# Kernel optimization log

Hardware: AMD Instinct MI355X
Metric: run time of the kernel (lower is better)

The kernel has to match this reference:

```python
import jax, jax.numpy as jnp
import numpy as np

MARGIN = 10.0
EPS = 1e-8


def setup_inputs() -> dict:
    key = jax.random.key(0)
    k1, k2, k3 = jax.random.split(key, 3)
    V, B, C, D = 2, 16384, 100, 512
    feat = jax.random.normal(k1, (V, B, D), dtype=jnp.float32)
    label = jax.random.randint(k2, (B,), 0, C, dtype=jnp.int64)
    anchor = jax.random.normal(k3, (V, C, D), dtype=jnp.float32)
    return {"feat": feat, "label": label, "anchor": anchor}


def reference(feat, label, anchor):
    # feat: [V, B, D], label: [B], anchor: [V, C, D]
    V, B, D = feat.shape
    C = anchor.shape[1]

    # ----- per-view center loss + cosine similarity -----
    centers = anchor[:, label, :]                      # [V, B, D] gather
    diff = feat - centers
    center_loss = jnp.sum(diff * diff, axis=(1, 2)) / 2.0 / B   # [V]

    fn = jnp.maximum(jnp.linalg.norm(feat, axis=-1), EPS)        # [V, B]
    cn = jnp.maximum(jnp.linalg.norm(centers, axis=-1), EPS)     # [V, B]
    sims = jnp.sum(feat * centers, axis=-1) / (fn * cn)          # [V, B]

    # ----- inter-class margin loss (vectorized pairwise sq-dist) -----
    sq = jnp.sum(anchor * anchor, axis=-1)             # [V, C]
    gram = jnp.einsum('vcd,ved->vce', anchor, anchor)  # [V, C, C]
    pd = sq[:, :, None] + sq[:, None, :] - 2.0 * gram  # [V, C, C] squared dists
    # sum over i<j = (full sum - diagonal) / 2; diagonal is 0 analytically
    diag = jnp.einsum('vcc->v', pd)
    pair_sum = (jnp.sum(pd, axis=(1, 2)) - diag) * 0.5            # [V]
    inter = pair_sum / (C * (C - 1))
    inter_loss = jnp.maximum(MARGIN - inter, 0.0)                 # [V]

    loss = jnp.mean(center_loss) + jnp.mean(inter_loss)
    return loss, sims
```

## Files before the change

### kernel.cpp

```cpp
#include <hip/hip_runtime.h>
#include <math.h>

namespace {
constexpr int V = 2;
constexpr int B = 16384;
constexpr int C = 100;
constexpr int D = 512;
constexpr float MARGIN = 10.0f;
constexpr float EPS = 1e-8f;

constexpr int RB = 2048;
constexpr int ROWS_PER_WAVE = 4;
constexpr int IB_PER_V = 8;
constexpr int IB = V * IB_PER_V;
constexpr int CHUNK = 13;
}

__global__ __launch_bounds__(256) void main_kernel(
    const float* __restrict__ feat, const int* __restrict__ label,
    const float* __restrict__ anchor, float* __restrict__ sims,
    float* __restrict__ ws)
{
    __shared__ float blk[4];
    const int wave = threadIdx.x >> 6;
    const int lane = threadIdx.x & 63;

    if (blockIdx.x < RB) {
        const int wid = blockIdx.x * 4 + wave;
        float s_dd = 0.f;
#pragma unroll
        for (int r = 0; r < ROWS_PER_WAVE; ++r) {
            const int row = wid * ROWS_PER_WAVE + r;
            const int v = row >> 14;
            const int b = row & (B - 1);
            const float* frow = feat + (size_t)row * D;
            const float* crow = anchor + ((size_t)v * C + label[b]) * D;
            float s_ff = 0.f, s_cc = 0.f, s_fc = 0.f;
#pragma unroll
            for (int h = 0; h < 2; ++h) {
                const int d = h * 256 + lane * 4;
                const float4 f = *reinterpret_cast<const float4*>(frow + d);
                const float4 c = *reinterpret_cast<const float4*>(crow + d);
                s_ff += f.x*f.x + f.y*f.y + f.z*f.z + f.w*f.w;
                s_cc += c.x*c.x + c.y*c.y + c.z*c.z + c.w*c.w;
                s_fc += f.x*c.x + f.y*c.y + f.z*c.z + f.w*c.w;
                const float dx = f.x-c.x, dy = f.y-c.y, dz = f.z-c.z, dw = f.w-c.w;
                s_dd += dx*dx + dy*dy + dz*dz + dw*dw;
            }
#pragma unroll
            for (int off = 32; off; off >>= 1) {
                s_ff += __shfl_xor(s_ff, off);
                s_cc += __shfl_xor(s_cc, off);
                s_fc += __shfl_xor(s_fc, off);
            }
            if (lane == 0) {
                const float fn = fmaxf(sqrtf(s_ff), EPS);
                const float cn = fmaxf(sqrtf(s_cc), EPS);
                sims[row] = s_fc / (fn * cn);
            }
        }
#pragma unroll
        for (int off = 32; off; off >>= 1) s_dd += __shfl_xor(s_dd, off);
        if (lane == 0) blk[wave] = s_dd;
        __syncthreads();
        if (threadIdx.x == 0)
            ws[blockIdx.x] = blk[0] + blk[1] + blk[2] + blk[3];
    } else {
        const int ib = blockIdx.x - RB;
        const int v = ib >> 3, chunk = ib & 7;
        const int c0 = chunk * CHUNK;
        const int c1 = (c0 + CHUNK < C) ? c0 + CHUNK : C;
        const float* a = anchor + (size_t)v * C * D;
        const int d0 = threadIdx.x, d1 = threadIdx.x + 256;
        float m0 = 0.f, m1 = 0.f, s = 0.f;
        for (int c = c0; c < c1; ++c) {
            const float x0 = a[(size_t)c * D + d0];
            const float x1 = a[(size_t)c * D + d1];
            m0 += x0; m1 += x1; s += x0*x0 + x1*x1;
        }
        float* im = ws + RB + IB;
        im[ib * D + d0] = m0;
        im[ib * D + d1] = m1;
#pragma unroll
        for (int off = 32; off; off >>= 1) s += __shfl_xor(s, off);
        if (lane == 0) blk[wave] = s;
        __syncthreads();
        if (threadIdx.x == 0)
            ws[RB + ib] = blk[0] + blk[1] + blk[2] + blk[3];
    }
}

__global__ __launch_bounds__(1024) void finalize_kernel(
    const float* __restrict__ ws, float* __restrict__ out)
{
    const float* partials = ws;
    const float* is = ws + RB;
    const float* im = ws + RB + IB;
    const int t = threadIdx.x;
    const int wave = t >> 6, lane = t & 63;

    float sdd = partials[t] + partials[t + 1024];

    const int v = t >> 9, d = t & 511;
    float m = 0.f;
#pragma unroll
    for (int k = 0; k < IB_PER_V; ++k)
        m += im[((size_t)v * IB_PER_V + k) * D + d];
    float mm = m * m;

#pragma unroll
    for (int off = 32; off; off >>= 1) {
        sdd += __shfl_xor(sdd, off);
        mm  += __shfl_xor(mm, off);
    }
    __shared__ float rdd[16], rmm[16];
    if (lane == 0) { rdd[wave] = sdd; rmm[wave] = mm; }
    __syncthreads();
    if (t == 0) {
        float ddt = 0.f;
        for (int w = 0; w < 16; ++w) ddt += rdd[w];
        float MM0 = 0.f, MM1 = 0.f;
        for (int w = 0; w < 8;  ++w) MM0 += rmm[w];
        for (int w = 8; w < 16; ++w) MM1 += rmm[w];
        float S0 = 0.f, S1 = 0.f;
        for (int k = 0; k < IB_PER_V; ++k) { S0 += is[k]; S1 += is[IB_PER_V + k]; }
        const float denom = (float)(C * (C - 1));
        const float inter0 = ((float)C * S0 - MM0) / denom;
        const float inter1 = ((float)C * S1 - MM1) / denom;
        const float il = 0.5f * (fmaxf(MARGIN - inter0, 0.f) +
                                 fmaxf(MARGIN - inter1, 0.f));
        out[0] = ddt / (4.0f * (float)B) + il;
    }
}

extern "C" void kernel_launch(void* const* d_in, const int* in_sizes, int n_in,
                              void* d_out, int out_size, void* d_ws, size_t ws_size,
                              hipStream_t stream)
{
    const float* feat   = (const float*)d_in[0];
    const int*   label  = (const int*)d_in[1];
    const float* anchor = (const float*)d_in[2];
    float* out  = (float*)d_out;
    float* ws   = (float*)d_ws;
    float* sims = out + 1;

    hipLaunchKernelGGL(main_kernel, dim3(RB + IB), dim3(256), 0, stream,
                       feat, label, anchor, sims, ws);
    hipLaunchKernelGGL(finalize_kernel, dim3(1), dim3(1024), 0, stream,
                       ws, out);
}
```

Before: 98.35 us.

## Fuse finalize into main kernel via last-block atomic counter

Removes the separate single-block finalize kernel. The last block to finish, detected with an atomic counter and threadfences, now performs the final reduction. The inter-class anchor-sum work moves onto the first 16 row blocks instead of running in extra blocks. This saves one kernel launch and the gap between kernels, but adds a memset launch for the counter and extra work on a few blocks.

Result: slower. 258.0 us (+162.3%).

```diff
diff --git a/kernel.cpp b/kernel.cpp
--- a/kernel.cpp
+++ b/kernel.cpp
@@ -9,64 +9,70 @@
 constexpr float MARGIN = 10.0f;
 constexpr float EPS = 1e-8f;
 
-constexpr int RB = 2048;
+constexpr int NB = 2048;
 constexpr int ROWS_PER_WAVE = 4;
 constexpr int IB_PER_V = 8;
 constexpr int IB = V * IB_PER_V;
 constexpr int CHUNK = 13;
+
+constexpr int WS_DD  = 0;
+constexpr int WS_S   = NB;
+constexpr int WS_M   = NB + IB;
+constexpr int WS_CNT = NB + IB + IB * D;
 }
 
 __global__ __launch_bounds__(256) void main_kernel(
     const float* __restrict__ feat, const int* __restrict__ label,
     const float* __restrict__ anchor, float* __restrict__ sims,
-    float* __restrict__ ws)
+    float* __restrict__ ws, unsigned* __restrict__ cnt,
+    float* __restrict__ out)
 {
     __shared__ float blk[4];
     const int wave = threadIdx.x >> 6;
     const int lane = threadIdx.x & 63;
 
-    if (blockIdx.x < RB) {
-        const int wid = blockIdx.x * 4 + wave;
-        float s_dd = 0.f;
+    const int wid = blockIdx.x * 4 + wave;
+    float s_dd = 0.f;
 #pragma unroll
-        for (int r = 0; r < ROWS_PER_WAVE; ++r) {
-            const int row = wid * ROWS_PER_WAVE + r;
-            const int v = row >> 14;
-            const int b = row & (B - 1);
-            const float* frow = feat + (size_t)row * D;
-            const float* crow = anchor + ((size_t)v * C + label[b]) * D;
-            float s_ff = 0.f, s_cc = 0.f, s_fc = 0.f;
+    for (int r = 0; r < ROWS_PER_WAVE; ++r) {
+        const int row = wid * ROWS_PER_WAVE + r;
+        const int v = row >> 14;
+        const int b = row & (B - 1);
+        const float* frow = feat + (size_t)row * D;
+        const float* crow = anchor + ((size_t)v * C + label[b]) * D;
+        float s_ff = 0.f, s_cc = 0.f, s_fc = 0.f;
 #pragma unroll
-            for (int h = 0; h < 2; ++h) {
-                const int d = h * 256 + lane * 4;
-                const float4 f = *reinterpret_cast<const float4*>(frow + d);
-                const float4 c = *reinterpret_cast<const float4*>(crow + d);
-                s_ff += f.x*f.x + f.y*f.y + f.z*f.z + f.w*f.w;
-                s_cc += c.x*c.x + c.y*c.y + c.z*c.z + c.w*c.w;
-                s_fc += f.x*c.x + f.y*c.y + f.z*c.z + f.w*c.w;
-                const float dx = f.x-c.x, dy = f.y-c.y, dz = f.z-c.z, dw = f.w-c.w;
-                s_dd += dx*dx + dy*dy + dz*dz + dw*dw;
-            }
-#pragma unroll
-            for (int off = 32; off; off >>= 1) {
-                s_ff += __shfl_xor(s_ff, off);
-                s_cc += __shfl_xor(s_cc, off);
-                s_fc += __shfl_xor(s_fc, off);
-            }
-            if (lane == 0) {
-                const float fn = fmaxf(sqrtf(s_ff), EPS);
-                const float cn = fmaxf(sqrtf(s_cc), EPS);
-                sims[row] = s_fc / (fn * cn);
-            }
+        for (int h = 0; h < 2; ++h) {
+            const int d = h * 256 + lane * 4;
+            const float4 f = *reinterpret_cast<const float4*>(frow + d);
+            const float4 c = *reinterpret_cast<const float4*>(crow + d);
+            s_ff += f.x*f.x + f.y*f.y + f.z*f.z + f.w*f.w;
+            s_cc += c.x*c.x + c.y*c.y + c.z*c.z + c.w*c.w;
+            s_fc += f.x*c.x + f.y*c.y + f.z*c.z + f.w*c.w;
+            const float dx = f.x-c.x, dy = f.y-c.y, dz = f.z-c.z, dw = f.w-c.w;
+            s_dd += dx*dx + dy*dy + dz*dz + dw*dw;
         }
 #pragma unroll
-        for (int off = 32; off; off >>= 1) s_dd += __shfl_xor(s_dd, off);
-        if (lane == 0) blk[wave] = s_dd;
-        __syncthreads();
-        if (threadIdx.x == 0)
-            ws[blockIdx.x] = blk[0] + blk[1] + blk[2] + blk[3];
-    } else {
-        const int ib = blockIdx.x - RB;
+        for (int off = 32; off; off >>= 1) {
+            s_ff += __shfl_xor(s_ff, off);
+            s_cc += __shfl_xor(s_cc, off);
+            s_fc += __shfl_xor(s_fc, off);
+        }
+        if (lane == 0) {
+            const float fn = fmaxf(sqrtf(s_ff), EPS);
+            const float cn = fmaxf(sqrtf(s_cc), EPS);
+            sims[row] = s_fc / (fn * cn);
+        }
+    }
+#pragma unroll
+    for (int off = 32; off; off >>= 1) s_dd += __shfl_xor(s_dd, off);
+    if (lane == 0) blk[wave] = s_dd;
+    __syncthreads();
+    if (threadIdx.x == 0)
+        ws[WS_DD + blockIdx.x] = blk[0] + blk[1] + blk[2] + blk[3];
+
+    if (blockIdx.x < IB) {
+        const int ib = blockIdx.x;
         const int v = ib >> 3, chunk = ib & 7;
         const int c0 = chunk * CHUNK;
         const int c1 = (c0 + CHUNK < C) ? c0 + CHUNK : C;
@@ -78,58 +84,64 @@
             const float x1 = a[(size_t)c * D + d1];
             m0 += x0; m1 += x1; s += x0*x0 + x1*x1;
         }
-        float* im = ws + RB + IB;
-        im[ib * D + d0] = m0;
-        im[ib * D + d1] = m1;
+        ws[WS_M + ib * D + d0] = m0;
+        ws[WS_M + ib * D + d1] = m1;
 #pragma unroll
         for (int off = 32; off; off >>= 1) s += __shfl_xor(s, off);
+        __syncthreads();
         if (lane == 0) blk[wave] = s;
         __syncthreads();
         if (threadIdx.x == 0)
-            ws[RB + ib] = blk[0] + blk[1] + blk[2] + blk[3];
+            ws[WS_S + ib] = blk[0] + blk[1] + blk[2] + blk[3];
     }
-}
 
-__global__ __launch_bounds__(1024) void finalize_kernel(
-    const float* __restrict__ ws, float* __restrict__ out)
-{
-    const float* partials = ws;
-    const float* is = ws + RB;
-    const float* im = ws + RB + IB;
-    const int t = threadIdx.x;
-    const int wave = t >> 6, lane = t & 63;
-
-    float sdd = partials[t] + partials[t + 1024];
-
-    const int v = t >> 9, d = t & 511;
-    float m = 0.f;
+    __threadfence();
+    __shared__ unsigned last;
+    if (threadIdx.x == 0) last = atomicAdd(cnt, 1u);
+    __syncthreads();
+    if (last == NB - 1) {
+        __threadfence();
+        const int t = threadIdx.x;
+        float sdd = 0.f;
 #pragma unroll
-    for (int k = 0; k < IB_PER_V; ++k)
-        m += im[((size_t)v * IB_PER_V + k) * D + d];
-    float mm = m * m;
-
+        for (int i = 0; i < 8; ++i) sdd += ws[WS_DD + t + i * 256];
+        float mm0 = 0.f, mm1 = 0.f;
 #pragma unroll
-    for (int off = 32; off; off >>= 1) {
-        sdd += __shfl_xor(sdd, off);
-        mm  += __shfl_xor(mm, off);
-    }
-    __shared__ float rdd[16], rmm[16];
-    if (lane == 0) { rdd[wave] = sdd; rmm[wave] = mm; }
-    __syncthreads();
-    if (t == 0) {
-        float ddt = 0.f;
-        for (int w = 0; w < 16; ++w) ddt += rdd[w];
-        float MM0 = 0.f, MM1 = 0.f;
-        for (int w = 0; w < 8;  ++w) MM0 += rmm[w];
-        for (int w = 8; w < 16; ++w) MM1 += rmm[w];
-        float S0 = 0.f, S1 = 0.f;
-        for (int k = 0; k < IB_PER_V; ++k) { S0 += is[k]; S1 += is[IB_PER_V + k]; }
-        const float denom = (float)(C * (C - 1));
-        const float inter0 = ((float)C * S0 - MM0) / denom;
-        const float inter1 = ((float)C * S1 - MM1) / denom;
-        const float il = 0.5f * (fmaxf(MARGIN - inter0, 0.f) +
-                                 fmaxf(MARGIN - inter1, 0.f));
-        out[0] = ddt / (4.0f * (float)B) + il;
+        for (int h = 0; h < 2; ++h) {
+            const int d = t + h * 256;
+            float m0 = 0.f, m1 = 0.f;
+#pragma unroll
+            for (int k = 0; k < IB_PER_V; ++k) {
+                m0 += ws[WS_M + (0 * IB_PER_V + k) * D + d];
+                m1 += ws[WS_M + (1 * IB_PER_V + k) * D + d];
+            }
+            mm0 += m0 * m0; mm1 += m1 * m1;
+        }
+#pragma unroll
+        for (int off = 32; off; off >>= 1) {
+            sdd += __shfl_xor(sdd, off);
+            mm0 += __shfl_xor(mm0, off);
+            mm1 += __shfl_xor(mm1, off);
+        }
+        __shared__ float rr[3][4];
+        if (lane == 0) { rr[0][wave] = sdd; rr[1][wave] = mm0; rr[2][wave] = mm1; }
+        __syncthreads();
+        if (t == 0) {
+            const float ddt = rr[0][0] + rr[0][1] + rr[0][2] + rr[0][3];
+            const float MM0 = rr[1][0] + rr[1][1] + rr[1][2] + rr[1][3];
+            const float MM1 = rr[2][0] + rr[2][1] + rr[2][2] + rr[2][3];
+            float S0 = 0.f, S1 = 0.f;
+            for (int k = 0; k < IB_PER_V; ++k) {
+                S0 += ws[WS_S + k];
+                S1 += ws[WS_S + IB_PER_V + k];
+            }
+            const float denom = (float)(C * (C - 1));
+            const float i0 = ((float)C * S0 - MM0) / denom;
+            const float i1 = ((float)C * S1 - MM1) / denom;
+            const float il = 0.5f * (fmaxf(MARGIN - i0, 0.f) +
+                                     fmaxf(MARGIN - i1, 0.f));
+            out[0] = ddt / (4.0f * (float)B) + il;
+        }
     }
 }
 
@@ -143,9 +155,9 @@
     float* out  = (float*)d_out;
     float* ws   = (float*)d_ws;
     float* sims = out + 1;
+    unsigned* cnt = (unsigned*)(ws + WS_CNT);
 
-    hipLaunchKernelGGL(main_kernel, dim3(RB + IB), dim3(256), 0, stream,
-                       feat, label, anchor, sims, ws);
-    hipLaunchKernelGGL(finalize_kernel, dim3(1), dim3(1024), 0, stream,
-                       ws, out);
+    hipMemsetAsync(cnt, 0, sizeof(unsigned), stream);
+    hipLaunchKernelGGL(main_kernel, dim3(NB), dim3(256), 0, stream,
+                       feat, label, anchor, sims, ws, cnt, out);
 }
```
